# Kernel optimization log

Measured on AMD Instinct MI355X. Metric: run time of the kernel, lower is better.

## Reference

```python
import jax, jax.numpy as jnp
import numpy as np

N_BOXES = 2048
N_CLASSES = 20


def _cross(a, b):
    return a[..., 0] * b[..., 1] - a[..., 1] * b[..., 0]


def _corners(box):
    # box: [5] = cx, cy, w, h, angle -> [4,2] corner coords
    cx, cy, w, h, a = box[0], box[1], box[2], box[3], box[4]
    c, s = jnp.cos(a), jnp.sin(a)
    dx = jnp.array([-1.0, 1.0, 1.0, -1.0], box.dtype) * (w * 0.5)
    dy = jnp.array([-1.0, -1.0, 1.0, 1.0], box.dtype) * (h * 0.5)
    return jnp.stack([cx + c * dx - s * dy, cy + s * dx + c * dy], axis=-1)


def _points_in_box(pts, box):
    # pts [K,2]; rotate into box frame, test axis-aligned containment
    cx, cy, w, h, a = box[0], box[1], box[2], box[3], box[4]
    c, s = jnp.cos(a), jnp.sin(a)
    px = pts[:, 0] - cx
    py = pts[:, 1] - cy
    lx = c * px + s * py
    ly = -s * px + c * py
    eps = 1e-5
    return (jnp.abs(lx) <= w * 0.5 + eps) & (jnp.abs(ly) <= h * 0.5 + eps)


def _pair_inter_area(box_a, box_b):
    # Exact convex intersection area of two rotated rectangles.
    ca = _corners(box_a)
    cb = _corners(box_b)
    # all 4x4 edge-pair intersections
    p = ca[:, None, :]
    r = (jnp.roll(ca, -1, 0) - ca)[:, None, :]
    q = cb[None, :, :]
    s_ = (jnp.roll(cb, -1, 0) - cb)[None, :, :]
    denom = _cross(r, s_)
    qp = q - p
    safe = jnp.where(jnp.abs(denom) > 1e-9, denom, 1.0)
    t = _cross(qp, s_) / safe
    u = _cross(qp, r) / safe
    valid_e = (jnp.abs(denom) > 1e-9) & (t >= 0.0) & (t <= 1.0) & (u >= 0.0) & (u <= 1.0)
    ipts = p + t[..., None] * r  # [4,4,2]
    # candidate polygon vertices: corners of A in B, corners of B in A, edge crossings
    pts = jnp.concatenate([ca, cb, ipts.reshape(16, 2)], axis=0)  # [24,2]
    mask = jnp.concatenate([_points_in_box(ca, box_b), _points_in_box(cb, box_a), valid_e.reshape(16)], axis=0)
    k = jnp.sum(mask)
    m = mask.astype(pts.dtype)[:, None]
    center = jnp.sum(pts * m, axis=0) / jnp.maximum(k, 1).astype(pts.dtype)
    d = pts - center
    ang = jnp.where(mask, jnp.arctan2(d[:, 1], d[:, 0]), 1e9)  # invalid -> sorted last
    idx = jnp.argsort(ang)
    ds = d[idx]
    ar = jnp.arange(24)
    nxt = jnp.where(ar + 1 < k, ar + 1, 0)
    cr = _cross(ds, ds[nxt])
    area = 0.5 * jnp.abs(jnp.sum(jnp.where(ar < k, cr, 0.0)))
    return jnp.where(k >= 3, area, 0.0)


def _iou_one_vs_many(box, boxes):
    inter = jax.vmap(lambda b: _pair_inter_area(box, b))(boxes)  # [N]
    area_a = box[2] * box[3]
    area_b = boxes[:, 2] * boxes[:, 3]
    return inter / (area_a + area_b - inter + 1e-9)


def _rotated_nms_mask(boxes, scores, iou_threshold):
    # sequential greedy suppression, highest score first; returns bool keep mask (original order)
    n = boxes.shape[0]
    order = jnp.argsort(-scores)
    bs = boxes[order]
    ar = jnp.arange(n)

    def body(i, keep):
        ious = _iou_one_vs_many(bs[i], bs)
        suppress = (ious > iou_threshold) & (ar > i) & keep[i]
        return keep & ~suppress

    keep_sorted = jax.lax.fori_loop(0, n, body, jnp.ones((n,), bool))
    return jnp.zeros((n,), bool).at[order].set(keep_sorted)


def setup_inputs() -> dict:
    key = jax.random.key(0)
    k1, k2, k3, k4, k5 = jax.random.split(key, 5)
    cxcy = jax.random.uniform(k1, (N_BOXES, 2), jnp.float32) * 1024.0
    wh = jax.random.uniform(k2, (N_BOXES, 2), jnp.float32) * 96.0 + 4.0
    ang = jax.random.uniform(k3, (N_BOXES, 1), jnp.float32) * np.pi
    boxes = jnp.concatenate([cxcy, wh, ang], axis=1)  # [N,5]
    scores = jax.random.uniform(k4, (N_BOXES,), jnp.float32)
    labels = jax.random.randint(k5, (N_BOXES,), 0, N_CLASSES, dtype=jnp.int64 if jax.config.read('jax_enable_x64') else jnp.int32)
    return {"boxes": boxes, "scores": scores, "labels": labels, "iou_threshold": 0.5}


def reference(boxes, scores, labels, iou_threshold):
    # multiclass NMS via coordinate-offset trick (N <= 20000 branch of forward)
    cx, cy, w, h = boxes[:, 0], boxes[:, 1], boxes[:, 2], boxes[:, 3]
    max_radius = jnp.max(jnp.sqrt(w * w + h * h)) * 0.5
    max_coord = jnp.maximum(jnp.max(cx), jnp.max(cy))
    offset_scale = (max_coord + max_radius) * 2.0 + 1.0
    offsets = labels.astype(boxes.dtype) * offset_scale
    boxes_nms = boxes.at[:, 0].add(offsets).at[:, 1].add(offsets)
    keep = _rotated_nms_mask(boxes_nms, scores, iou_threshold)
    # fixed-shape encoding of the kept-index set: score of kept boxes, 0 for suppressed
    return scores * keep.astype(scores.dtype)
```

## Files before the change

kernel.cpp:

```cpp
#include <hip/hip_runtime.h>
#include <cstdint>

typedef unsigned long long u64;
typedef uint32_t u32;

#define NB 2048
#define EDGE_CAP 16384
#define CLIST_CAP 2048

__global__ __launch_bounds__(256) void build_kernel(
    const float* __restrict__ boxes, const float* __restrict__ scores,
    const int* __restrict__ labels,
    float* __restrict__ cxp, float* __restrict__ cyp, float* __restrict__ wp,
    float* __restrict__ hp, float* __restrict__ cp, float* __restrict__ sp,
    float* __restrict__ radp, float* __restrict__ sscp, int* __restrict__ sidx,
    u32* __restrict__ counters) {
#pragma clang fp contract(off)
  __shared__ float sc[NB];
  __shared__ float smc[4], smr[4];
  int t = threadIdx.x;
  if (blockIdx.x == 0 && t < 4) counters[t] = 0u;
  float mc = -1e30f, mr = -1e30f;
  for (int k = t; k < NB; k += 256) {
    float cx = boxes[k * 5 + 0];
    float cy = boxes[k * 5 + 1];
    float w = boxes[k * 5 + 2];
    float h = boxes[k * 5 + 3];
    mc = fmaxf(mc, fmaxf(cx, cy));
    float ww = w * w;
    float hh = h * h;
    mr = fmaxf(mr, sqrtf(ww + hh));
    sc[k] = scores[k];
  }
  for (int off = 32; off > 0; off >>= 1) {
    mc = fmaxf(mc, __shfl_down(mc, off));
    mr = fmaxf(mr, __shfl_down(mr, off));
  }
  if ((t & 63) == 0) { smc[t >> 6] = mc; smr[t >> 6] = mr; }
  __syncthreads();
  mc = fmaxf(fmaxf(smc[0], smc[1]), fmaxf(smc[2], smc[3]));
  mr = fmaxf(fmaxf(smr[0], smr[1]), fmaxf(smr[2], smr[3]));
  float osc = (mc + mr * 0.5f) * 2.0f + 1.0f;

  int wave = t >> 6, lane = t & 63;
  int i = blockIdx.x * 4 + wave;
  float si = sc[i];
  int rank = 0;
#pragma unroll 8
  for (int m = 0; m < NB / 64; ++m) {
    int j = m * 64 + lane;
    float sj = sc[j];
    rank += (int)((sj > si) || (sj == si && j < i));
  }
  for (int off = 32; off > 0; off >>= 1) rank += __shfl_down(rank, off);
  if (lane == 0) {
    float off = (float)labels[i] * osc;
    float cx = boxes[i * 5 + 0] + off;
    float cy = boxes[i * 5 + 1] + off;
    float w = boxes[i * 5 + 2];
    float h = boxes[i * 5 + 3];
    float a = boxes[i * 5 + 4];
    float c = cosf(a);
    float s = sinf(a);
    float ww = w * w;
    float hh = h * h;
    cxp[rank] = cx;
    cyp[rank] = cy;
    wp[rank] = w;
    hp[rank] = h;
    cp[rank] = c;
    sp[rank] = s;
    radp[rank] = 0.5f * sqrtf(ww + hh);
    sscp[rank] = si;
    sidx[rank] = i;
  }
}

__global__ __launch_bounds__(256) void candgeom_greedy_kernel(
    const float* __restrict__ cxp, const float* __restrict__ cyp,
    const float* __restrict__ wp, const float* __restrict__ hp,
    const float* __restrict__ cp, const float* __restrict__ sp,
    const float* __restrict__ radp, const float* __restrict__ thrp,
    const float* __restrict__ sscp, const int* __restrict__ sidx,
    u32* __restrict__ edges, u32* __restrict__ counters,
    float* __restrict__ out) {
#pragma clang fp contract(off)
  __shared__ float lx[NB], ly[NB], lr[NB];
  __shared__ u32 clist[CLIST_CAP];
  __shared__ float dxL[256 * 25];
  __shared__ float dyL[256 * 25];
  __shared__ u32 ccnt;
  __shared__ int is_last;
  __shared__ u64 keepw[32];
  __shared__ u32 Sw32[64];
  __shared__ int changed;
  int t = threadIdx.x;
  if (t == 0) ccnt = 0;
  for (int k = t; k < NB; k += 256) {
    lx[k] = cxp[k];
    ly[k] = cyp[k];
    lr[k] = radp[k];
  }
  __syncthreads();
  int i0 = blockIdx.x * 8;
#pragma unroll
  for (int di = 0; di < 8; ++di) {
    int i = i0 + di;
    float ax = lx[i], ay = ly[i], ar = lr[i];
#pragma unroll
    for (int c = 0; c < 8; ++c) {
      int j = c * 256 + t;
      if (j > i) {
        float dx = lx[j] - ax, dy = ly[j] - ay;
        float rr = ar + lr[j] + 1.0f;
        if (dx * dx + dy * dy <= rr * rr) {
          u32 s = atomicAdd(&ccnt, 1u);
          if (s < CLIST_CAP) clist[s] = ((u32)i << 16) | (u32)j;
        }
      }
    }
  }
  __syncthreads();
  u32 cnt = ccnt < CLIST_CAP ? ccnt : CLIST_CAP;
  float thr = *thrp;
  float* myDx = &dxL[t * 25];
  float* myDy = &dyL[t * 25];
  for (u32 idx = t; idx < cnt; idx += 256) {
    u32 pk = clist[idx];
    int bi = (int)(pk >> 16);
    int bj = (int)(pk & 0xFFFFu);
    float acx = lx[bi], acy = ly[bi], aw = wp[bi], ah = hp[bi];
    float ac = cp[bi], as_ = sp[bi];
    float bcx = lx[bj], bcy = ly[bj], bw = wp[bj], bh = hp[bj];
    float bc = cp[bj], bs_ = sp[bj];
    const float SX[4] = {-1.f, 1.f, 1.f, -1.f};
    const float SY[4] = {-1.f, -1.f, 1.f, 1.f};
    float axx[4], ayy[4], bxx[4], byy[4];
    float ahw = aw * 0.5f, ahh = ah * 0.5f;
    float bhw = bw * 0.5f, bhh = bh * 0.5f;
#pragma unroll
    for (int q = 0; q < 4; ++q) {
      float dx = SX[q] * ahw, dy = SY[q] * ahh;
      axx[q] = acx + ac * dx - as_ * dy;
      ayy[q] = acy + as_ * dx + ac * dy;
      float ex = SX[q] * bhw, ey = SY[q] * bhh;
      bxx[q] = bcx + bc * ex - bs_ * ey;
      byy[q] = bcy + bs_ * ex + bc * ey;
    }
    float px_[24], py_[24];
    bool mk[24];
#pragma unroll
    for (int q = 0; q < 4; ++q) {
      {
        float axp = axx[q] - bcx, ayp = ayy[q] - bcy;
        float lxx = bc * axp + bs_ * ayp;
        float lyy = bc * ayp - bs_ * axp;
        mk[q] = (fabsf(lxx) <= bhw + 1e-5f) && (fabsf(lyy) <= bhh + 1e-5f);
        px_[q] = axx[q]; py_[q] = ayy[q];
      }
      {
        float axp = bxx[q] - acx, ayp = byy[q] - acy;
        float lxx = ac * axp + as_ * ayp;
        float lyy = ac * ayp - as_ * axp;
        mk[4 + q] = (fabsf(lxx) <= ahw + 1e-5f) && (fabsf(lyy) <= ahh + 1e-5f);
        px_[4 + q] = bxx[q]; py_[4 + q] = byy[q];
      }
    }
#pragma unroll
    for (int e = 0; e < 4; ++e) {
      float rx = axx[(e + 1) & 3] - axx[e];
      float ry = ayy[(e + 1) & 3] - ayy[e];
#pragma unroll
      for (int f = 0; f < 4; ++f) {
        float sx = bxx[(f + 1) & 3] - bxx[f];
        float sy = byy[(f + 1) & 3] - byy[f];
        float denom = rx * sy - ry * sx;
        float qpx = bxx[f] - axx[e];
        float qpy = byy[f] - ayy[e];
        bool dn = fabsf(denom) > 1e-9f;
        float safe = dn ? denom : 1.0f;
        float tt = (qpx * sy - qpy * sx) / safe;
        float uu = (qpx * ry - qpy * rx) / safe;
        bool valid = dn && (tt >= 0.0f) && (tt <= 1.0f) && (uu >= 0.0f) && (uu <= 1.0f);
        int id = 8 + e * 4 + f;
        px_[id] = axx[e] + tt * rx;
        py_[id] = ayy[e] + tt * ry;
        mk[id] = valid;
      }
    }
    int k = 0;
    float sx0 = 0.0f, sy0 = 0.0f;
#pragma unroll
    for (int q = 0; q < 24; ++q) {
      if (mk[q]) { k++; sx0 += px_[q]; sy0 += py_[q]; }
    }
    float kkf = (float)(k > 0 ? k : 1);
    float cxm = sx0 / kkf, cym = sy0 / kkf;
    u64 key[32];
#pragma unroll
    for (int q = 0; q < 24; ++q) {
      float dx = px_[q] - cxm, dy = py_[q] - cym;
      myDx[q] = dx; myDy[q] = dy;
      float sm = fabsf(dx) + fabsf(dy);
      float r = (sm > 0.0f) ? dy / sm : 0.0f;
      float pa;
      if (dx >= 0.0f) pa = r;
      else pa = (__float_as_uint(dy) >> 31) ? (-2.0f - r) : (2.0f - r);
      float ang = mk[q] ? pa : 1e9f;
      u32 ub = __float_as_uint(ang);
      u32 v = (ub & 0x80000000u) ? ~ub : (ub | 0x80000000u);
      key[q] = (((u64)v) << 5) | (u64)q;
    }
#pragma unroll
    for (int q = 24; q < 32; ++q) key[q] = ~0ull;
#pragma unroll
    for (int kk2 = 2; kk2 <= 32; kk2 <<= 1) {
#pragma unroll
      for (int jj = kk2 >> 1; jj > 0; jj >>= 1) {
#pragma unroll
        for (int ii = 0; ii < 32; ++ii) {
          int ll = ii ^ jj;
          if (ll > ii) {
            bool up = ((ii & kk2) == 0);
            u64 ka = key[ii], kb = key[ll];
            bool sw = up ? (ka > kb) : (ka < kb);
            key[ii] = sw ? kb : ka;
            key[ll] = sw ? ka : kb;
          }
        }
      }
    }
    float acc = 0.0f;
    int id0 = (int)(key[0] & 31ull);
    float fx = myDx[id0], fy = myDy[id0];
    float curx = fx, cury = fy;
#pragma unroll
    for (int q = 0; q < 24; ++q) {
      if (q < k - 1) {
        int idn = (int)(key[q + 1] & 31ull);
        float nx = myDx[idn], ny = myDy[idn];
        acc += curx * ny - cury * nx;
        curx = nx; cury = ny;
      } else if (q == k - 1) {
        acc += curx * fy - cury * fx;
      }
    }
    float area = 0.5f * fabsf(acc);
    float inter = (k >= 3) ? area : 0.0f;
    float areaA = aw * ah;
    float areaB = bw * bh;
    float iou = inter / (areaA + areaB - inter + 1e-9f);
    if (iou > thr) {
      u32 e = atomicAdd(&counters[1], 1u);
      if (e < EDGE_CAP) edges[e] = pk;
    }
  }
  __syncthreads();
  if (t == 0) {
    __threadfence();
    u32 old = atomicAdd(&counters[2], 1u);
    is_last = (old == (u32)(gridDim.x - 1)) ? 1 : 0;
  }
  __syncthreads();
  if (!is_last) return;
  __threadfence();
  __syncthreads();
  u32 ecnt = counters[1];
  if (ecnt > EDGE_CAP) ecnt = EDGE_CAP;
  u32 nl = ecnt < CLIST_CAP ? ecnt : CLIST_CAP;
  for (u32 k = t; k < nl; k += 256) clist[k] = edges[k];
  if (t < 32) keepw[t] = ~0ull;
  __syncthreads();
  for (int iter = 0; iter < 2060; ++iter) {
    if (t < 64) Sw32[t] = 0u;
    if (t == 0) changed = 0;
    __syncthreads();
    for (u32 k = t; k < ecnt; k += 256) {
      u32 pk = (k < CLIST_CAP) ? clist[k] : edges[k];
      int i = (int)(pk >> 16);
      int j = (int)(pk & 0xFFFFu);
      if ((keepw[i >> 6] >> (i & 63)) & 1ull)
        atomicOr(&Sw32[j >> 5], 1u << (j & 31));
    }
    __syncthreads();
    if (t < 32) {
      u64 S = ((u64)Sw32[2 * t]) | (((u64)Sw32[2 * t + 1]) << 32);
      u64 nk = ~S;
      if (nk != keepw[t]) { keepw[t] = nk; changed = 1; }
    }
    __syncthreads();
    int ch = changed;
    __syncthreads();
    if (!ch) break;
  }
  for (int p = t; p < NB; p += 256) {
    int bit = (int)((keepw[p >> 6] >> (p & 63)) & 1ull);
    out[sidx[p]] = bit ? sscp[p] : 0.0f;
  }
}

extern "C" void kernel_launch(void* const* d_in, const int* in_sizes, int n_in,
                              void* d_out, int out_size, void* d_ws, size_t ws_size,
                              hipStream_t stream) {
  const float* boxes = (const float*)d_in[0];
  const float* scores = (const float*)d_in[1];
  const int* labels = (const int*)d_in[2];
  const float* thr = (const float*)d_in[3];
  float* out = (float*)d_out;

  char* base = (char*)d_ws;
  u32* counters = (u32*)base;
  float* arr = (float*)(base + 256);
  float* cxp = arr + 0 * NB;
  float* cyp = arr + 1 * NB;
  float* wp = arr + 2 * NB;
  float* hp = arr + 3 * NB;
  float* cp = arr + 4 * NB;
  float* sp = arr + 5 * NB;
  float* radp = arr + 6 * NB;
  float* sscp = arr + 7 * NB;
  int* sidx = (int*)(base + 66048);
  u32* edges = (u32*)(base + 81920);

  build_kernel<<<512, 256, 0, stream>>>(boxes, scores, labels, cxp, cyp, wp, hp,
                                        cp, sp, radp, sscp, sidx, counters);
  candgeom_greedy_kernel<<<256, 256, 0, stream>>>(cxp, cyp, wp, hp, cp, sp,
                                                  radp, thr, sscp, sidx,
                                                  edges, counters, out);
}
```

Measured before the change: 88.78 us.

## Fuse build and candidate/greedy kernels into one cooperative kernel with grid syncs

Merges the sort/build kernel and the candidate-geometry/greedy kernel into a single cooperative launch of 256 blocks. Each block now ranks 8 boxes instead of 4. Two grid-wide syncs replace the kernel boundary and the last-block atomic detection. This removes one kernel launch and the inter-kernel gap. In exchange it adds the cost of cooperative launch and grid barriers, and it needs all 256 blocks, with their large shared-memory footprint, to be co-resident.

```diff
diff --git a/kernel.cpp b/kernel.cpp
--- a/kernel.cpp
+++ b/kernel.cpp
@@ -1,5 +1,8 @@
 #include <hip/hip_runtime.h>
+#include <hip/hip_cooperative_groups.h>
 #include <cstdint>
+
+namespace cg = cooperative_groups;
 
 typedef unsigned long long u64;
 typedef uint32_t u32;
@@ -8,18 +11,32 @@
 #define EDGE_CAP 16384
 #define CLIST_CAP 2048
 
-__global__ __launch_bounds__(256) void build_kernel(
+__global__ __launch_bounds__(256) void nms_all_kernel(
     const float* __restrict__ boxes, const float* __restrict__ scores,
-    const int* __restrict__ labels,
+    const int* __restrict__ labels, const float* __restrict__ thrp,
     float* __restrict__ cxp, float* __restrict__ cyp, float* __restrict__ wp,
     float* __restrict__ hp, float* __restrict__ cp, float* __restrict__ sp,
     float* __restrict__ radp, float* __restrict__ sscp, int* __restrict__ sidx,
-    u32* __restrict__ counters) {
+    u32* __restrict__ edges, u32* __restrict__ counters,
+    float* __restrict__ out) {
 #pragma clang fp contract(off)
-  __shared__ float sc[NB];
+  cg::grid_group grid = cg::this_grid();
+  __shared__ float lx[NB], ly[NB], lr[NB];
+  __shared__ u32 clist[CLIST_CAP];
+  __shared__ float dxL[256 * 25];
+  __shared__ float dyL[256 * 25];
   __shared__ float smc[4], smr[4];
+  __shared__ u32 ccnt;
+  __shared__ u64 keepw[32];
+  __shared__ u32 Sw32[64];
+  __shared__ int changed;
+
   int t = threadIdx.x;
-  if (blockIdx.x == 0 && t < 4) counters[t] = 0u;
+  int b = blockIdx.x;
+  int wave = t >> 6, lane = t & 63;
+
+  if (b == 0 && t < 4) counters[t] = 0u;
+  float* sc = lx;
   float mc = -1e30f, mr = -1e30f;
   for (int k = t; k < NB; k += 256) {
     float cx = boxes[k * 5 + 0];
@@ -42,59 +59,43 @@
   mr = fmaxf(fmaxf(smr[0], smr[1]), fmaxf(smr[2], smr[3]));
   float osc = (mc + mr * 0.5f) * 2.0f + 1.0f;
 
-  int wave = t >> 6, lane = t & 63;
-  int i = blockIdx.x * 4 + wave;
-  float si = sc[i];
-  int rank = 0;
+#pragma unroll
+  for (int rep = 0; rep < 2; ++rep) {
+    int i = b * 8 + rep * 4 + wave;
+    float si = sc[i];
+    int rank = 0;
 #pragma unroll 8
-  for (int m = 0; m < NB / 64; ++m) {
-    int j = m * 64 + lane;
-    float sj = sc[j];
-    rank += (int)((sj > si) || (sj == si && j < i));
-  }
-  for (int off = 32; off > 0; off >>= 1) rank += __shfl_down(rank, off);
-  if (lane == 0) {
-    float off = (float)labels[i] * osc;
-    float cx = boxes[i * 5 + 0] + off;
-    float cy = boxes[i * 5 + 1] + off;
-    float w = boxes[i * 5 + 2];
-    float h = boxes[i * 5 + 3];
-    float a = boxes[i * 5 + 4];
-    float c = cosf(a);
-    float s = sinf(a);
-    float ww = w * w;
-    float hh = h * h;
-    cxp[rank] = cx;
-    cyp[rank] = cy;
-    wp[rank] = w;
-    hp[rank] = h;
-    cp[rank] = c;
-    sp[rank] = s;
-    radp[rank] = 0.5f * sqrtf(ww + hh);
-    sscp[rank] = si;
-    sidx[rank] = i;
-  }
-}
-
-__global__ __launch_bounds__(256) void candgeom_greedy_kernel(
-    const float* __restrict__ cxp, const float* __restrict__ cyp,
-    const float* __restrict__ wp, const float* __restrict__ hp,
-    const float* __restrict__ cp, const float* __restrict__ sp,
-    const float* __restrict__ radp, const float* __restrict__ thrp,
-    const float* __restrict__ sscp, const int* __restrict__ sidx,
-    u32* __restrict__ edges, u32* __restrict__ counters,
-    float* __restrict__ out) {
-#pragma clang fp contract(off)
-  __shared__ float lx[NB], ly[NB], lr[NB];
-  __shared__ u32 clist[CLIST_CAP];
-  __shared__ float dxL[256 * 25];
-  __shared__ float dyL[256 * 25];
-  __shared__ u32 ccnt;
-  __shared__ int is_last;
-  __shared__ u64 keepw[32];
-  __shared__ u32 Sw32[64];
-  __shared__ int changed;
-  int t = threadIdx.x;
+    for (int m = 0; m < NB / 64; ++m) {
+      int j = m * 64 + lane;
+      float sj = sc[j];
+      rank += (int)((sj > si) || (sj == si && j < i));
+    }
+    for (int off = 32; off > 0; off >>= 1) rank += __shfl_down(rank, off);
+    if (lane == 0) {
+      float off = (float)labels[i] * osc;
+      float cx = boxes[i * 5 + 0] + off;
+      float cy = boxes[i * 5 + 1] + off;
+      float w = boxes[i * 5 + 2];
+      float h = boxes[i * 5 + 3];
+      float a = boxes[i * 5 + 4];
+      float c = cosf(a);
+      float s = sinf(a);
+      float ww = w * w;
+      float hh = h * h;
+      cxp[rank] = cx;
+      cyp[rank] = cy;
+      wp[rank] = w;
+      hp[rank] = h;
+      cp[rank] = c;
+      sp[rank] = s;
+      radp[rank] = 0.5f * sqrtf(ww + hh);
+      sscp[rank] = si;
+      sidx[rank] = i;
+    }
+  }
+  __threadfence();
+  grid.sync();
+
   if (t == 0) ccnt = 0;
   for (int k = t; k < NB; k += 256) {
     lx[k] = cxp[k];
@@ -102,7 +103,7 @@
     lr[k] = radp[k];
   }
   __syncthreads();
-  int i0 = blockIdx.x * 8;
+  int i0 = b * 8;
 #pragma unroll
   for (int di = 0; di < 8; ++di) {
     int i = i0 + di;
@@ -255,16 +256,10 @@
       if (e < EDGE_CAP) edges[e] = pk;
     }
   }
-  __syncthreads();
-  if (t == 0) {
-    __threadfence();
-    u32 old = atomicAdd(&counters[2], 1u);
-    is_last = (old == (u32)(gridDim.x - 1)) ? 1 : 0;
-  }
-  __syncthreads();
-  if (!is_last) return;
   __threadfence();
-  __syncthreads();
+  grid.sync();
+
+  if (b != 0) return;
   u32 ecnt = counters[1];
   if (ecnt > EDGE_CAP) ecnt = EDGE_CAP;
   u32 nl = ecnt < CLIST_CAP ? ecnt : CLIST_CAP;
@@ -322,9 +317,10 @@
   int* sidx = (int*)(base + 66048);
   u32* edges = (u32*)(base + 81920);
 
-  build_kernel<<<512, 256, 0, stream>>>(boxes, scores, labels, cxp, cyp, wp, hp,
-                                        cp, sp, radp, sscp, sidx, counters);
-  candgeom_greedy_kernel<<<256, 256, 0, stream>>>(cxp, cyp, wp, hp, cp, sp,
-                                                  radp, thr, sscp, sidx,
-                                                  edges, counters, out);
+  void* args[] = {(void*)&boxes, (void*)&scores, (void*)&labels, (void*)&thr,
+                  (void*)&cxp, (void*)&cyp, (void*)&wp, (void*)&hp,
+                  (void*)&cp, (void*)&sp, (void*)&radp, (void*)&sscp,
+                  (void*)&sidx, (void*)&edges, (void*)&counters, (void*)&out};
+  hipLaunchCooperativeKernel((const void*)nms_all_kernel, dim3(256), dim3(256),
+                             args, 0, stream);
 }
```

Measured after the change: 171.5 us. 93.1% more time.

## Pack center/radius as float4, drop LDS staging, and double candidate-kernel grid

Applied to the files above, without the earlier changes.

Build kernel now writes a packed float4 (cx, cy, radius) per sorted box. The candidate kernel no longer stages all 2048 boxes into shared memory; each thread keeps its 8 j-boxes in registers and reads the i-box directly as a float4. The grid doubles to 512 blocks with 4 rows each, which spreads the pair test and per-block greedy work over more blocks. Pair geometry now reads centers from global memory instead of LDS, and the workspace layout is reshuffled.

```diff
diff --git a/kernel.cpp b/kernel.cpp
--- a/kernel.cpp
+++ b/kernel.cpp
@@ -7,13 +7,14 @@
 #define NB 2048
 #define EDGE_CAP 16384
 #define CLIST_CAP 2048
+
 
 __global__ __launch_bounds__(256) void build_kernel(
     const float* __restrict__ boxes, const float* __restrict__ scores,
     const int* __restrict__ labels,
     float* __restrict__ cxp, float* __restrict__ cyp, float* __restrict__ wp,
     float* __restrict__ hp, float* __restrict__ cp, float* __restrict__ sp,
-    float* __restrict__ radp, float* __restrict__ sscp, int* __restrict__ sidx,
+    float4* __restrict__ pxyr, float* __restrict__ sscp, int* __restrict__ sidx,
     u32* __restrict__ counters) {
 #pragma clang fp contract(off)
   __shared__ float sc[NB];
@@ -64,13 +65,14 @@
     float s = sinf(a);
     float ww = w * w;
     float hh = h * h;
+    float rad = 0.5f * sqrtf(ww + hh);
     cxp[rank] = cx;
     cyp[rank] = cy;
     wp[rank] = w;
     hp[rank] = h;
     cp[rank] = c;
     sp[rank] = s;
-    radp[rank] = 0.5f * sqrtf(ww + hh);
+    pxyr[rank] = make_float4(cx, cy, rad, 0.0f);
     sscp[rank] = si;
     sidx[rank] = i;
   }
@@ -80,12 +82,11 @@
     const float* __restrict__ cxp, const float* __restrict__ cyp,
     const float* __restrict__ wp, const float* __restrict__ hp,
     const float* __restrict__ cp, const float* __restrict__ sp,
-    const float* __restrict__ radp, const float* __restrict__ thrp,
+    const float4* __restrict__ pxyr, const float* __restrict__ thrp,
     const float* __restrict__ sscp, const int* __restrict__ sidx,
     u32* __restrict__ edges, u32* __restrict__ counters,
     float* __restrict__ out) {
 #pragma clang fp contract(off)
-  __shared__ float lx[NB], ly[NB], lr[NB];
   __shared__ u32 clist[CLIST_CAP];
   __shared__ float dxL[256 * 25];
   __shared__ float dyL[256 * 25];
@@ -96,23 +97,25 @@
   __shared__ int changed;
   int t = threadIdx.x;
   if (t == 0) ccnt = 0;
-  for (int k = t; k < NB; k += 256) {
-    lx[k] = cxp[k];
-    ly[k] = cyp[k];
-    lr[k] = radp[k];
-  }
-  __syncthreads();
-  int i0 = blockIdx.x * 8;
-#pragma unroll
-  for (int di = 0; di < 8; ++di) {
+  float jx[8], jy[8], jr[8];
+#pragma unroll
+  for (int c = 0; c < 8; ++c) {
+    float4 v = pxyr[c * 256 + t];
+    jx[c] = v.x; jy[c] = v.y; jr[c] = v.z;
+  }
+  __syncthreads();
+  int i0 = blockIdx.x * 4;
+#pragma unroll
+  for (int di = 0; di < 4; ++di) {
     int i = i0 + di;
-    float ax = lx[i], ay = ly[i], ar = lr[i];
+    float4 pi = pxyr[i];
+    float ax = pi.x, ay = pi.y, ar = pi.z;
 #pragma unroll
     for (int c = 0; c < 8; ++c) {
       int j = c * 256 + t;
       if (j > i) {
-        float dx = lx[j] - ax, dy = ly[j] - ay;
-        float rr = ar + lr[j] + 1.0f;
+        float dx = jx[c] - ax, dy = jy[c] - ay;
+        float rr = ar + jr[c] + 1.0f;
         if (dx * dx + dy * dy <= rr * rr) {
           u32 s = atomicAdd(&ccnt, 1u);
           if (s < CLIST_CAP) clist[s] = ((u32)i << 16) | (u32)j;
@@ -129,9 +132,9 @@
     u32 pk = clist[idx];
     int bi = (int)(pk >> 16);
     int bj = (int)(pk & 0xFFFFu);
-    float acx = lx[bi], acy = ly[bi], aw = wp[bi], ah = hp[bi];
+    float acx = cxp[bi], acy = cyp[bi], aw = wp[bi], ah = hp[bi];
     float ac = cp[bi], as_ = sp[bi];
-    float bcx = lx[bj], bcy = ly[bj], bw = wp[bj], bh = hp[bj];
+    float bcx = cxp[bj], bcy = cyp[bj], bw = wp[bj], bh = hp[bj];
     float bc = cp[bj], bs_ = sp[bj];
     const float SX[4] = {-1.f, 1.f, 1.f, -1.f};
     const float SY[4] = {-1.f, -1.f, 1.f, 1.f};
@@ -317,14 +320,14 @@
   float* hp = arr + 3 * NB;
   float* cp = arr + 4 * NB;
   float* sp = arr + 5 * NB;
-  float* radp = arr + 6 * NB;
-  float* sscp = arr + 7 * NB;
-  int* sidx = (int*)(base + 66048);
-  u32* edges = (u32*)(base + 81920);
+  float* sscp = arr + 6 * NB;
+  int* sidx = (int*)(base + 57600);
+  float4* pxyr = (float4*)(base + 66048);
+  u32* edges = (u32*)(base + 102400);
 
   build_kernel<<<512, 256, 0, stream>>>(boxes, scores, labels, cxp, cyp, wp, hp,
-                                        cp, sp, radp, sscp, sidx, counters);
-  candgeom_greedy_kernel<<<256, 256, 0, stream>>>(cxp, cyp, wp, hp, cp, sp,
-                                                  radp, thr, sscp, sidx,
+                                        cp, sp, pxyr, sscp, sidx, counters);
+  candgeom_greedy_kernel<<<512, 256, 0, stream>>>(cxp, cyp, wp, hp, cp, sp,
+                                                  pxyr, thr, sscp, sidx,
                                                   edges, counters, out);
 }
```

Result: no change. 88.42 us (median of 2 runs) (-0.4%).
